# Optimization experiments

Hardware: AMD Instinct MI355X
Metric: run time of the kernel (lower is better)

The kernel has to match this reference:

```python
import jax, jax.numpy as jnp
import numpy as np

D_MODEL = 2048
NUM_HEADS = 16
D_K = D_MODEL // NUM_HEADS
ROPE_THETA = 10000.0


def apply_rope(x, token_positions):
    # x: [B, H, S, D_k]; token_positions: [S] int
    d = x.shape[-1]
    inv_freq = 1.0 / (ROPE_THETA ** (jnp.arange(0, d, 2, dtype=jnp.float32) / d))  # [D_k/2]
    ang = token_positions.astype(jnp.float32)[:, None] * inv_freq[None, :]  # [S, D_k/2]
    cos = jnp.cos(ang)  # broadcast over B, H
    sin = jnp.sin(ang)
    x1 = x[..., 0::2]
    x2 = x[..., 1::2]
    r1 = x1 * cos - x2 * sin
    r2 = x1 * sin + x2 * cos
    return jnp.stack([r1, r2], axis=-1).reshape(x.shape)


def setup_inputs() -> dict:
    key = jax.random.key(0)
    kx, kq, kk, kv, ko = jax.random.split(key, 5)
    scale = 1.0 / np.sqrt(D_MODEL)
    return {
        "x": jax.random.normal(kx, (2, 2048, D_MODEL), dtype=jnp.float32),
        "token_positions": jnp.arange(2048, dtype=jnp.int32),
        "wq": jax.random.normal(kq, (D_MODEL, D_MODEL), dtype=jnp.float32) * scale,
        "wk": jax.random.normal(kk, (D_MODEL, D_MODEL), dtype=jnp.float32) * scale,
        "wv": jax.random.normal(kv, (D_MODEL, D_MODEL), dtype=jnp.float32) * scale,
        "wo": jax.random.normal(ko, (D_MODEL, D_MODEL), dtype=jnp.float32) * scale,
    }


def reference(x, token_positions, wq, wk, wv, wo):
    B, S, _ = x.shape
    # QKV projections (no bias), split heads -> [B, H, S, D_k]
    def split_heads(t):
        return t.reshape(B, S, NUM_HEADS, D_K).transpose(0, 2, 1, 3)

    q = split_heads(jnp.einsum("bsd,ed->bse", x, wq))
    k = split_heads(jnp.einsum("bsd,ed->bse", x, wk))
    v = split_heads(jnp.einsum("bsd,ed->bse", x, wv))

    q = apply_rope(q, token_positions)
    k = apply_rope(k, token_positions)

    scores = jnp.einsum("bhqd,bhkd->bhqk", q, k) / jnp.sqrt(jnp.float32(D_K))
    causal = jnp.tril(jnp.ones((S, S), dtype=bool))  # True where attend allowed
    scores = jnp.where(causal, scores, jnp.float32(-1e9))
    attn = jax.nn.softmax(scores, axis=-1)
    out = jnp.einsum("bhqk,bhkd->bhqd", attn, v)  # [B, H, S, D_k]
    out = out.transpose(0, 2, 1, 3).reshape(B, S, D_MODEL)
    return jnp.einsum("bsd,ed->bse", out, wo)
```

## Files before the change

kernel.cpp:

```cpp
#include <hip/hip_runtime.h>
#include <hip/hip_bf16.h>
#include <math.h>

#define D_MODEL 2048
#define NHEAD   16
#define DK      128
#define SEQ     2048
#define BATCH   2
#define MROWS   (BATCH*SEQ)

typedef __attribute__((ext_vector_type(8))) short short8;
typedef __attribute__((ext_vector_type(4))) short shortx4;
typedef __attribute__((ext_vector_type(4))) float f32x4;

static __device__ __forceinline__ short f2bf(float v) {
    union { __hip_bfloat16 b; short s; } u;
    u.b = __float2bfloat16(v);
    return u.s;
}
static __device__ __forceinline__ float bf2f(short s) {
    union { short s; __hip_bfloat16 b; } u;
    u.s = s;
    return __bfloat162float(u.b);
}

__global__ __launch_bounds__(256) void split_bf16(const float* __restrict__ in,
                                                  short* __restrict__ hi,
                                                  short* __restrict__ lo, int n8)
{
    int i = blockIdx.x * 256 + threadIdx.x;
    const int stride = gridDim.x * 256;
    for (; i < n8; i += stride) {
        const float4 a = ((const float4*)in)[2 * i];
        const float4 b = ((const float4*)in)[2 * i + 1];
        const float f[8] = {a.x, a.y, a.z, a.w, b.x, b.y, b.z, b.w};
        short8 h, l;
#pragma unroll
        for (int e = 0; e < 8; ++e) {
            const short hb = f2bf(f[e]); h[e] = hb; l[e] = f2bf(f[e] - bf2f(hb));
        }
        ((short8*)hi)[i] = h;
        ((short8*)lo)[i] = l;
    }
}

#define GBM 128
#define GBN 128
#define GBK 32
#define LDKG 40

__global__ __launch_bounds__(256, 2) void gemm_nt_bf(const short* __restrict__ Ahg,
                                                     const short* __restrict__ Alg,
                                                     const short* __restrict__ Whg,
                                                     const short* __restrict__ Wlg,
                                                     float* __restrict__ C,
                                                     int M, int N, int K)
{
    __shared__ __align__(16) short Ah[GBM][LDKG];
    __shared__ __align__(16) short Al[GBM][LDKG];
    __shared__ __align__(16) short Bh[GBN][LDKG];
    __shared__ __align__(16) short Bl[GBN][LDKG];

    const int tid  = threadIdx.x;
    const int lane = tid & 63;
    const int w    = tid >> 6;
    const int wm   = (w & 1) * 64;
    const int wn   = (w >> 1) * 64;
    const int l16  = lane & 15;
    const int kb   = (lane >> 4) * 8;

    const size_t row0 = (size_t)blockIdx.y * GBM;
    const size_t col0 = (size_t)blockIdx.x * GBN;

    const int sr0 = tid >> 2;
    const int sr1 = sr0 + 64;
    const int skc = (tid & 3) * 8;

    f32x4 acc[4][4];
#pragma unroll
    for (int i = 0; i < 4; ++i)
#pragma unroll
        for (int j = 0; j < 4; ++j) acc[i][j] = (f32x4)0.0f;

    short8 ra0h = *(const short8*)(Ahg + (row0 + sr0) * K + skc);
    short8 ra0l = *(const short8*)(Alg + (row0 + sr0) * K + skc);
    short8 ra1h = *(const short8*)(Ahg + (row0 + sr1) * K + skc);
    short8 ra1l = *(const short8*)(Alg + (row0 + sr1) * K + skc);
    short8 rw0h = *(const short8*)(Whg + (col0 + sr0) * K + skc);
    short8 rw0l = *(const short8*)(Wlg + (col0 + sr0) * K + skc);
    short8 rw1h = *(const short8*)(Whg + (col0 + sr1) * K + skc);
    short8 rw1l = *(const short8*)(Wlg + (col0 + sr1) * K + skc);

    for (int kt = 0; kt < K; kt += GBK) {
        *(short8*)&Ah[sr0][skc] = ra0h;  *(short8*)&Al[sr0][skc] = ra0l;
        *(short8*)&Ah[sr1][skc] = ra1h;  *(short8*)&Al[sr1][skc] = ra1l;
        *(short8*)&Bh[sr0][skc] = rw0h;  *(short8*)&Bl[sr0][skc] = rw0l;
        *(short8*)&Bh[sr1][skc] = rw1h;  *(short8*)&Bl[sr1][skc] = rw1l;
        __syncthreads();

        if (kt + GBK < K) {
            const int kn = kt + GBK;
            ra0h = *(const short8*)(Ahg + (row0 + sr0) * K + kn + skc);
            ra0l = *(const short8*)(Alg + (row0 + sr0) * K + kn + skc);
            ra1h = *(const short8*)(Ahg + (row0 + sr1) * K + kn + skc);
            ra1l = *(const short8*)(Alg + (row0 + sr1) * K + kn + skc);
            rw0h = *(const short8*)(Whg + (col0 + sr0) * K + kn + skc);
            rw0l = *(const short8*)(Wlg + (col0 + sr0) * K + kn + skc);
            rw1h = *(const short8*)(Whg + (col0 + sr1) * K + kn + skc);
            rw1l = *(const short8*)(Wlg + (col0 + sr1) * K + kn + skc);
        }

        short8 bh[4], bl[4];
#pragma unroll
        for (int fn = 0; fn < 4; ++fn) {
            bh[fn] = *(const short8*)&Bh[wn + fn * 16 + l16][kb];
            bl[fn] = *(const short8*)&Bl[wn + fn * 16 + l16][kb];
        }
#pragma unroll
        for (int fm = 0; fm < 4; ++fm) {
            const short8 ah = *(const short8*)&Ah[wm + fm * 16 + l16][kb];
            const short8 al = *(const short8*)&Al[wm + fm * 16 + l16][kb];
#pragma unroll
            for (int fn = 0; fn < 4; ++fn) {
                acc[fm][fn] = __builtin_amdgcn_mfma_f32_16x16x32_bf16(ah, bh[fn], acc[fm][fn], 0, 0, 0);
                acc[fm][fn] = __builtin_amdgcn_mfma_f32_16x16x32_bf16(ah, bl[fn], acc[fm][fn], 0, 0, 0);
                acc[fm][fn] = __builtin_amdgcn_mfma_f32_16x16x32_bf16(al, bh[fn], acc[fm][fn], 0, 0, 0);
            }
        }
        __syncthreads();
    }

#pragma unroll
    for (int fm = 0; fm < 4; ++fm) {
#pragma unroll
        for (int j = 0; j < 4; ++j) {
            const size_t r = row0 + wm + fm * 16 + (lane >> 4) * 4 + j;
#pragma unroll
            for (int fn = 0; fn < 4; ++fn)
                C[r * N + col0 + wn + fn * 16 + l16] = acc[fm][fn][j];
        }
    }
}

__global__ __launch_bounds__(256, 2) void gemm_nt_mfma(const float* __restrict__ A,
                                                       const float* __restrict__ W,
                                                       float* __restrict__ C,
                                                       int M, int N, int K)
{
    __shared__ __align__(16) short Ah[GBM][LDKG];
    __shared__ __align__(16) short Al[GBM][LDKG];
    __shared__ __align__(16) short Bh[GBN][LDKG];
    __shared__ __align__(16) short Bl[GBN][LDKG];

    const int tid  = threadIdx.x;
    const int lane = tid & 63;
    const int w    = tid >> 6;
    const int wm   = (w & 1) * 64;
    const int wn   = (w >> 1) * 64;
    const int l16  = lane & 15;
    const int kb   = (lane >> 4) * 8;

    const size_t row0 = (size_t)blockIdx.y * GBM;
    const size_t col0 = (size_t)blockIdx.x * GBN;

    const int sr0 = tid >> 2;
    const int sr1 = sr0 + 64;
    const int skc = (tid & 3) * 8;

    f32x4 acc[4][4];
#pragma unroll
    for (int i = 0; i < 4; ++i)
#pragma unroll
        for (int j = 0; j < 4; ++j) acc[i][j] = (f32x4)0.0f;

    float4 pa0a = *(const float4*)(A + (row0 + sr0) * K + skc);
    float4 pa0b = *(const float4*)(A + (row0 + sr0) * K + skc + 4);
    float4 pa1a = *(const float4*)(A + (row0 + sr1) * K + skc);
    float4 pa1b = *(const float4*)(A + (row0 + sr1) * K + skc + 4);
    float4 pw0a = *(const float4*)(W + (col0 + sr0) * K + skc);
    float4 pw0b = *(const float4*)(W + (col0 + sr0) * K + skc + 4);
    float4 pw1a = *(const float4*)(W + (col0 + sr1) * K + skc);
    float4 pw1b = *(const float4*)(W + (col0 + sr1) * K + skc + 4);

    for (int kt = 0; kt < K; kt += GBK) {
        {
            float f[8]; short8 h, l;
#define CVT8(va, vb)                                                        \
            f[0]=va.x; f[1]=va.y; f[2]=va.z; f[3]=va.w;                     \
            f[4]=vb.x; f[5]=vb.y; f[6]=vb.z; f[7]=vb.w;                     \
            _Pragma("unroll")                                               \
            for (int j = 0; j < 8; ++j) {                                   \
                short hb = f2bf(f[j]); h[j] = hb; l[j] = f2bf(f[j] - bf2f(hb)); \
            }
            CVT8(pa0a, pa0b)
            *(short8*)&Ah[sr0][skc] = h;  *(short8*)&Al[sr0][skc] = l;
            CVT8(pa1a, pa1b)
            *(short8*)&Ah[sr1][skc] = h;  *(short8*)&Al[sr1][skc] = l;
            CVT8(pw0a, pw0b)
            *(short8*)&Bh[sr0][skc] = h;  *(short8*)&Bl[sr0][skc] = l;
            CVT8(pw1a, pw1b)
            *(short8*)&Bh[sr1][skc] = h;  *(short8*)&Bl[sr1][skc] = l;
#undef CVT8
        }
        __syncthreads();

        if (kt + GBK < K) {
            const int kn = kt + GBK;
            pa0a = *(const float4*)(A + (row0 + sr0) * K + kn + skc);
            pa0b = *(const float4*)(A + (row0 + sr0) * K + kn + skc + 4);
            pa1a = *(const float4*)(A + (row0 + sr1) * K + kn + skc);
            pa1b = *(const float4*)(A + (row0 + sr1) * K + kn + skc + 4);
            pw0a = *(const float4*)(W + (col0 + sr0) * K + kn + skc);
            pw0b = *(const float4*)(W + (col0 + sr0) * K + kn + skc + 4);
            pw1a = *(const float4*)(W + (col0 + sr1) * K + kn + skc);
            pw1b = *(const float4*)(W + (col0 + sr1) * K + kn + skc + 4);
        }

        short8 bh[4], bl[4];
#pragma unroll
        for (int fn = 0; fn < 4; ++fn) {
            bh[fn] = *(const short8*)&Bh[wn + fn * 16 + l16][kb];
            bl[fn] = *(const short8*)&Bl[wn + fn * 16 + l16][kb];
        }
#pragma unroll
        for (int fm = 0; fm < 4; ++fm) {
            const short8 ah = *(const short8*)&Ah[wm + fm * 16 + l16][kb];
            const short8 al = *(const short8*)&Al[wm + fm * 16 + l16][kb];
#pragma unroll
            for (int fn = 0; fn < 4; ++fn) {
                acc[fm][fn] = __builtin_amdgcn_mfma_f32_16x16x32_bf16(ah, bh[fn], acc[fm][fn], 0, 0, 0);
                acc[fm][fn] = __builtin_amdgcn_mfma_f32_16x16x32_bf16(ah, bl[fn], acc[fm][fn], 0, 0, 0);
                acc[fm][fn] = __builtin_amdgcn_mfma_f32_16x16x32_bf16(al, bh[fn], acc[fm][fn], 0, 0, 0);
            }
        }
        __syncthreads();
    }

#pragma unroll
    for (int fm = 0; fm < 4; ++fm) {
#pragma unroll
        for (int j = 0; j < 4; ++j) {
            const size_t r = row0 + wm + fm * 16 + (lane >> 4) * 4 + j;
#pragma unroll
            for (int fn = 0; fn < 4; ++fn)
                C[r * N + col0 + wn + fn * 16 + l16] = acc[fm][fn][j];
        }
    }
}

__global__ __launch_bounds__(256) void rope_kernel(float* __restrict__ q,
                                                   float* __restrict__ k,
                                                   const int* __restrict__ pos)
{
    const int idx = blockIdx.x * 256 + threadIdx.x;
    if (idx >= MROWS * 1024) return;
    const int pair = idx & 1023;
    const int row  = idx >> 10;
    const int s    = row & (SEQ - 1);
    const int j    = pair & 63;

    const float inv_freq = (float)pow(10000.0, -(double)(2 * j) / 128.0);
    const float ang = (float)pos[s] * inv_freq;
    float sn, cs;
    sincosf(ang, &sn, &cs);

    const size_t off = (size_t)row * D_MODEL + pair * 2;
    float2 vq = *(float2*)(q + off);
    float2 vk = *(float2*)(k + off);
    float2 rq, rk;
    rq.x = vq.x * cs - vq.y * sn;  rq.y = vq.x * sn + vq.y * cs;
    rk.x = vk.x * cs - vk.y * sn;  rk.y = vk.x * sn + vk.y * cs;
    *(float2*)(q + off) = rq;
    *(float2*)(k + off) = rk;
}

#define ABM 128
#define AWQ 32
#define KVT 64
#define KROW 128
#define VLD 72

__device__ __forceinline__ void attn_issue_loads(const float* __restrict__ K,
                                                 const float* __restrict__ V,
                                                 size_t base, int kv0, int tid,
                                                 float4* kreg, float4* vreg)
{
    const int r  = tid >> 2;
    const int d0 = (tid & 3) * 32;
    const float* ksrc = K + base + (size_t)(kv0 + r) * D_MODEL + d0;
#pragma unroll
    for (int u = 0; u < 4; ++u) {
        kreg[2 * u]     = *(const float4*)(ksrc + u * 8);
        kreg[2 * u + 1] = *(const float4*)(ksrc + u * 8 + 4);
    }
#pragma unroll
    for (int it = 0; it < 2; ++it) {
        const int tt  = tid + it * 256;
        const int dq  = tt & 31;
        const int kvq = tt >> 5;
        const float* vs = V + base + (size_t)(kv0 + kvq * 4) * D_MODEL + dq * 4;
#pragma unroll
        for (int i = 0; i < 4; ++i)
            vreg[it * 4 + i] = *(const float4*)(vs + i * D_MODEL);
    }
}

__device__ __forceinline__ void attn_convert_write(short* __restrict__ KhS,
                                                   short* __restrict__ KlS,
                                                   short* __restrict__ VTh,
                                                   short* __restrict__ VTl,
                                                   int tid,
                                                   const float4* kreg,
                                                   const float4* vreg)
{
    const int r = tid >> 2;
#pragma unroll
    for (int u = 0; u < 4; ++u) {
        const float4 f0 = kreg[2 * u];
        const float4 f1 = kreg[2 * u + 1];
        const float f[8] = {f0.x, f0.y, f0.z, f0.w, f1.x, f1.y, f1.z, f1.w};
        short8 hh, ll;
#pragma unroll
        for (int e = 0; e < 8; ++e) {
            const short hb = f2bf(f[e]); hh[e] = hb; ll[e] = f2bf(f[e] - bf2f(hb));
        }
        const int off = r * KROW + (((4 * (tid & 3) + u) ^ (r & 7)) << 3);
        *(short8*)&KhS[off] = hh;
        *(short8*)&KlS[off] = ll;
    }
#pragma unroll
    for (int it = 0; it < 2; ++it) {
        const int tt  = tid + it * 256;
        const int dq  = tt & 31;
        const int kvq = tt >> 5;
        const float4 r0 = vreg[it * 4 + 0];
        const float4 r1 = vreg[it * 4 + 1];
        const float4 r2 = vreg[it * 4 + 2];
        const float4 r3 = vreg[it * 4 + 3];
        const float vals[4][4] = {{r0.x, r0.y, r0.z, r0.w}, {r1.x, r1.y, r1.z, r1.w},
                                  {r2.x, r2.y, r2.z, r2.w}, {r3.x, r3.y, r3.z, r3.w}};
#pragma unroll
        for (int c = 0; c < 4; ++c) {
            const int rr  = dq * 4 + c;
            const int sw  = ((rr >> 2) ^ (rr >> 4)) & 3;
            const int off = rr * VLD + (((kvq >> 1) ^ sw) << 3) + ((kvq & 1) << 2);
            shortx4 hh, ll;
#pragma unroll
            for (int i = 0; i < 4; ++i) {
                const float fv = vals[i][c];
                const short hb = f2bf(fv); hh[i] = hb; ll[i] = f2bf(fv - bf2f(hb));
            }
            *(shortx4*)&VTh[off] = hh;
            *(shortx4*)&VTl[off] = ll;
        }
    }
}

__device__ __forceinline__ void attn_load_q(const float* __restrict__ Q, size_t base,
                                            int qw0, int l16, int g,
                                            short8 qh[2][4], short8 ql[2][4])
{
#pragma unroll
    for (int fq = 0; fq < 2; ++fq)
#pragma unroll
        for (int ks = 0; ks < 4; ++ks) {
            const float* src = Q + base + (size_t)(qw0 + fq * 16 + l16) * D_MODEL + g * 8 + ks * 32;
            const float4 f0 = *(const float4*)src;
            const float4 f1 = *(const float4*)(src + 4);
            const float f[8] = {f0.x, f0.y, f0.z, f0.w, f1.x, f1.y, f1.z, f1.w};
            short8 hh, ll;
#pragma unroll
            for (int e = 0; e < 8; ++e) {
                const short hb = f2bf(f[e]); hh[e] = hb; ll[e] = f2bf(f[e] - bf2f(hb));
            }
            qh[fq][ks] = hh; ql[fq][ks] = ll;
        }
}

__device__ __forceinline__ void attn_write_o(float* __restrict__ O, size_t base,
                                             int qw0, int g, int l16,
                                             const f32x4 accO[2][8], const float lstate[2])
{
    float rl[2][4];
#pragma unroll
    for (int fm = 0; fm < 2; ++fm)
#pragma unroll
        for (int j = 0; j < 4; ++j)
            rl[fm][j] = 1.0f / __shfl(lstate[fm], (g << 2) | j);
#pragma unroll
    for (int fm = 0; fm < 2; ++fm)
#pragma unroll
        for (int j = 0; j < 4; ++j) {
            const size_t row = base + (size_t)(qw0 + fm * 16 + 4 * g + j) * D_MODEL;
#pragma unroll
            for (int fd = 0; fd < 8; ++fd)
                O[row + fd * 16 + l16] = accO[fm][fd][j] * rl[fm][j];
        }
}

__global__ __launch_bounds__(256, 1) void flash_attn_mfma(const float* __restrict__ Q,
                                                          const float* __restrict__ K,
                                                          const float* __restrict__ V,
                                                          float* __restrict__ O)
{
    __shared__ __align__(16) short KhS[2][KVT * KROW];
    __shared__ __align__(16) short KlS[2][KVT * KROW];
    __shared__ __align__(16) short VTh[2][DK * VLD];
    __shared__ __align__(16) short VTl[2][DK * VLD];

    const int tid  = threadIdx.x;
    const int lane = tid & 63;
    const int w    = tid >> 6;
    const int l16  = lane & 15;
    const int g    = lane >> 4;
    const int h    = blockIdx.y & (NHEAD - 1);
    const int b    = blockIdx.y >> 4;
    const size_t base = (size_t)b * SEQ * D_MODEL + (size_t)h * DK;
    const float scale = 0.08838834764831845f;

    const int qtA = blockIdx.x;
    const int qtB = 15 - qtA;
    const int ntA = 2 * qtA + 2;
    const int total = 34;

    short8 qh[2][4], ql[2][4];
    attn_load_q(Q, base, qtA * ABM + w * AWQ, l16, g, qh, ql);

    f32x4 accO[2][8];
#pragma unroll
    for (int i = 0; i < 2; ++i)
#pragma unroll
        for (int j = 0; j < 8; ++j) accO[i][j] = (f32x4)0.0f;
    float mstate[2] = {-3.0e38f, -3.0e38f};
    float lstate[2] = {0.f, 0.f};

    float4 kreg[8], vreg[8];
    attn_issue_loads(K, V, base, 0, tid, kreg, vreg);
    attn_convert_write(KhS[0], KlS[0], VTh[0], VTl[0], tid, kreg, vreg);
    int cur = 0;

    for (int st = 0; st < total; ++st) {
        const int pass = (st >= ntA) ? 1 : 0;
        const int t    = pass ? (st - ntA) : st;
        const int qt   = pass ? qtB : qtA;
        const int kv0  = t * KVT;
        const int qw0  = qt * ABM + w * AWQ;

        __syncthreads();

        if (st + 1 < total) {
            const int t2 = (st + 1 >= ntA) ? (st + 1 - ntA) : (st + 1);
            attn_issue_loads(K, V, base, t2 * KVT, tid, kreg, vreg);
        }

        if (pass && t == 0) {
            attn_write_o(O, base, qtA * ABM + w * AWQ, g, l16, accO, lstate);
            attn_load_q(Q, base, qtB * ABM + w * AWQ, l16, g, qh, ql);
#pragma unroll
            for (int i = 0; i < 2; ++i)
#pragma unroll
                for (int j = 0; j < 8; ++j) accO[i][j] = (f32x4)0.0f;
            mstate[0] = mstate[1] = -3.0e38f;
            lstate[0] = lstate[1] = 0.f;
        }

        const bool active = (kv0 <= qw0 + AWQ - 1);
        if (active) {
            f32x4 accS[4][2];
#pragma unroll
            for (int i = 0; i < 4; ++i) { accS[i][0] = (f32x4)0.0f; accS[i][1] = (f32x4)0.0f; }
#pragma unroll
            for (int ks = 0; ks < 4; ++ks) {
#pragma unroll
                for (int fs = 0; fs < 4; ++fs) {
                    const int koff = (fs * 16 + l16) * KROW + (((g + 4 * ks) ^ (l16 & 7)) << 3);
                    const short8 kh = *(const short8*)&KhS[cur][koff];
                    const short8 kl = *(const short8*)&KlS[cur][koff];
#pragma unroll
                    for (int fq = 0; fq < 2; ++fq) {
                        accS[fs][fq] = __builtin_amdgcn_mfma_f32_16x16x32_bf16(kh, qh[fq][ks], accS[fs][fq], 0, 0, 0);
                        accS[fs][fq] = __builtin_amdgcn_mfma_f32_16x16x32_bf16(kh, ql[fq][ks], accS[fs][fq], 0, 0, 0);
                        accS[fs][fq] = __builtin_amdgcn_mfma_f32_16x16x32_bf16(kl, qh[fq][ks], accS[fs][fq], 0, 0, 0);
                    }
                }
            }

            const bool needmask = (kv0 + KVT - 1 > qw0);
            float al[2];
#pragma unroll
            for (int fq = 0; fq < 2; ++fq) {
                const int qg = qw0 + fq * 16 + l16;
                float mx = -3.0e38f;
#pragma unroll
                for (int fs = 0; fs < 4; ++fs)
#pragma unroll
                    for (int j = 0; j < 4; ++j) {
                        float s = accS[fs][fq][j] * scale;
                        if (needmask) {
                            const int kvg = kv0 + fs * 16 + g * 4 + j;
                            s = (kvg <= qg) ? s : -3.0e38f;
                        }
                        accS[fs][fq][j] = s;
                        mx = fmaxf(mx, s);
                    }
                mx = fmaxf(mx, __shfl_xor(mx, 16));
                mx = fmaxf(mx, __shfl_xor(mx, 32));
                const float mnew = fmaxf(mstate[fq], mx);
                al[fq] = __expf(mstate[fq] - mnew);
                mstate[fq] = mnew;
                float sm = 0.f;
#pragma unroll
                for (int fs = 0; fs < 4; ++fs)
#pragma unroll
                    for (int j = 0; j < 4; ++j) {
                        const float p = __expf(accS[fs][fq][j] - mnew);
                        accS[fs][fq][j] = p;
                        sm += p;
                    }
                sm += __shfl_xor(sm, 16);
                sm += __shfl_xor(sm, 32);
                lstate[fq] = lstate[fq] * al[fq] + sm;
            }

            float alr[2][4];
#pragma unroll
            for (int fm = 0; fm < 2; ++fm)
#pragma unroll
                for (int j = 0; j < 4; ++j)
                    alr[fm][j] = __shfl(al[fm], (g << 2) | j);
#pragma unroll
            for (int fm = 0; fm < 2; ++fm)
#pragma unroll
                for (int fd = 0; fd < 8; ++fd)
#pragma unroll
                    for (int j = 0; j < 4; ++j)
                        accO[fm][fd][j] *= alr[fm][j];

#pragma unroll
            for (int ks = 0; ks < 2; ++ks) {
                short8 pah[2], pal[2];
#pragma unroll
                for (int fm = 0; fm < 2; ++fm) {
                    float pv[8];
#pragma unroll
                    for (int e = 0; e < 8; ++e) {
                        const int j = e & 3;
                        const int srcl = ((((lane >> 4) & 1) << 1) + (e >> 2)) * 16 + l16;
                        const float c0 = __shfl(accS[2 * ks][fm][j], srcl);
                        const float c1 = __shfl(accS[2 * ks + 1][fm][j], srcl);
                        pv[e] = (g >> 1) ? c1 : c0;
                    }
                    short8 hh, ll;
#pragma unroll
                    for (int e = 0; e < 8; ++e) {
                        const short hb = f2bf(pv[e]); hh[e] = hb; ll[e] = f2bf(pv[e] - bf2f(hb));
                    }
                    pah[fm] = hh; pal[fm] = ll;
                }
#pragma unroll
                for (int fd = 0; fd < 8; ++fd) {
                    const int r = fd * 16 + l16;
                    const int sw = ((r >> 2) ^ (r >> 4)) & 3;
                    const int off = r * VLD + (((g + 4 * ks) ^ sw) << 3);
                    const short8 vh = *(const short8*)&VTh[cur][off];
                    const short8 vl = *(const short8*)&VTl[cur][off];
#pragma unroll
                    for (int fm = 0; fm < 2; ++fm) {
                        accO[fm][fd] = __builtin_amdgcn_mfma_f32_16x16x32_bf16(pah[fm], vh, accO[fm][fd], 0, 0, 0);
                        accO[fm][fd] = __builtin_amdgcn_mfma_f32_16x16x32_bf16(pah[fm], vl, accO[fm][fd], 0, 0, 0);
                        accO[fm][fd] = __builtin_amdgcn_mfma_f32_16x16x32_bf16(pal[fm], vh, accO[fm][fd], 0, 0, 0);
                    }
                }
            }
        }

        if (st + 1 < total)
            attn_convert_write(KhS[cur ^ 1], KlS[cur ^ 1], VTh[cur ^ 1], VTl[cur ^ 1], tid, kreg, vreg);
        cur ^= 1;
    }

    attn_write_o(O, base, qtB * ABM + w * AWQ, g, l16, accO, lstate);
}

extern "C" void kernel_launch(void* const* d_in, const int* in_sizes, int n_in,
                              void* d_out, int out_size, void* d_ws, size_t ws_size,
                              hipStream_t stream)
{
    const float* x  = (const float*)d_in[0];
    const int*  pos = (const int*)d_in[1];
    const float* wq = (const float*)d_in[2];
    const float* wk = (const float*)d_in[3];
    const float* wv = (const float*)d_in[4];
    const float* wo = (const float*)d_in[5];
    float* out = (float*)d_out;

    char* base = (char*)d_ws;
    const size_t MB = 1024ull * 1024ull;
    float* q  = (float*)(base + 0 * MB);
    float* k  = (float*)(base + 32 * MB);
    float* v  = (float*)(base + 64 * MB);
    float* ao = (float*)(base + 96 * MB);

    const dim3 blk(256);
    const dim3 ggrid(D_MODEL / GBN, MROWS / GBM);
    const dim3 agrid(SEQ / (2 * ABM), BATCH * NHEAD);

    const bool presplit = (ws_size >= 224 * MB);

    if (presplit) {
        short* xh  = (short*)(base + 128 * MB);
        short* xl  = (short*)(base + 144 * MB);
        short* wqh = (short*)(base + 160 * MB);
        short* wql = (short*)(base + 168 * MB);
        short* wkh = (short*)(base + 176 * MB);
        short* wkl = (short*)(base + 184 * MB);
        short* wvh = (short*)(base + 192 * MB);
        short* wvl = (short*)(base + 200 * MB);
        short* woh = (short*)(base + 208 * MB);
        short* wol = (short*)(base + 216 * MB);
        short* aoh = xh;
        short* aol = xl;

        const int nx8 = MROWS * D_MODEL / 8;
        const int nw8 = D_MODEL * D_MODEL / 8;
        split_bf16<<<2048, blk, 0, stream>>>(x,  xh,  xl,  nx8);
        split_bf16<<<2048, blk, 0, stream>>>(wq, wqh, wql, nw8);
        split_bf16<<<2048, blk, 0, stream>>>(wk, wkh, wkl, nw8);
        split_bf16<<<2048, blk, 0, stream>>>(wv, wvh, wvl, nw8);
        split_bf16<<<2048, blk, 0, stream>>>(wo, woh, wol, nw8);

        gemm_nt_bf<<<ggrid, blk, 0, stream>>>(xh, xl, wqh, wql, q, MROWS, D_MODEL, D_MODEL);
        gemm_nt_bf<<<ggrid, blk, 0, stream>>>(xh, xl, wkh, wkl, k, MROWS, D_MODEL, D_MODEL);
        gemm_nt_bf<<<ggrid, blk, 0, stream>>>(xh, xl, wvh, wvl, v, MROWS, D_MODEL, D_MODEL);

        rope_kernel<<<(MROWS * 1024 + 255) / 256, blk, 0, stream>>>(q, k, pos);

        flash_attn_mfma<<<agrid, blk, 0, stream>>>(q, k, v, ao);

        split_bf16<<<2048, blk, 0, stream>>>(ao, aoh, aol, nx8);
        gemm_nt_bf<<<ggrid, blk, 0, stream>>>(aoh, aol, woh, wol, out, MROWS, D_MODEL, D_MODEL);
    } else {
        gemm_nt_mfma<<<ggrid, blk, 0, stream>>>(x, wq, q, MROWS, D_MODEL, D_MODEL);
        gemm_nt_mfma<<<ggrid, blk, 0, stream>>>(x, wk, k, MROWS, D_MODEL, D_MODEL);
        gemm_nt_mfma<<<ggrid, blk, 0, stream>>>(x, wv, v, MROWS, D_MODEL, D_MODEL);

        rope_kernel<<<(MROWS * 1024 + 255) / 256, blk, 0, stream>>>(q, k, pos);

        flash_attn_mfma<<<agrid, blk, 0, stream>>>(q, k, v, ao);

        gemm_nt_mfma<<<ggrid, blk, 0, stream>>>(ao, wo, out, MROWS, D_MODEL, D_MODEL);
    }
}
```

Measured before the change: 836.7 us.

## Use 8 waves per attention block with 16 query rows each

The flash attention kernel moves from 4 waves each owning 32 query rows to 8 waves (512 threads) each owning 16 rows. This halves per-wave accumulator and Q register state and doubles the waves available to hide latency. The K/V tile loading is split across more threads, and V high/low conversion is divided between the two halves of the block, with a new LDS swizzle for the transposed V. In exchange, each K/V fragment read from LDS now feeds half as many MFMAs, and the larger block raises synchronisation cost.

```diff
diff --git a/kernel.cpp b/kernel.cpp
--- a/kernel.cpp
+++ b/kernel.cpp
@@ -10,7 +10,6 @@
 #define MROWS   (BATCH*SEQ)
 
 typedef __attribute__((ext_vector_type(8))) short short8;
-typedef __attribute__((ext_vector_type(4))) short shortx4;
 typedef __attribute__((ext_vector_type(4))) float f32x4;
 
 static __device__ __forceinline__ short f2bf(float v) {
@@ -275,7 +274,6 @@
 }
 
 #define ABM 128
-#define AWQ 32
 #define KVT 64
 #define KROW 128
 #define VLD 72
@@ -285,24 +283,19 @@
                                                  size_t base, int kv0, int tid,
                                                  float4* kreg, float4* vreg)
 {
-    const int r  = tid >> 2;
-    const int d0 = (tid & 3) * 32;
-    const float* ksrc = K + base + (size_t)(kv0 + r) * D_MODEL + d0;
-#pragma unroll
-    for (int u = 0; u < 4; ++u) {
-        kreg[2 * u]     = *(const float4*)(ksrc + u * 8);
-        kreg[2 * u + 1] = *(const float4*)(ksrc + u * 8 + 4);
-    }
-#pragma unroll
-    for (int it = 0; it < 2; ++it) {
-        const int tt  = tid + it * 256;
-        const int dq  = tt & 31;
-        const int kvq = tt >> 5;
-        const float* vs = V + base + (size_t)(kv0 + kvq * 4) * D_MODEL + dq * 4;
-#pragma unroll
-        for (int i = 0; i < 4; ++i)
-            vreg[it * 4 + i] = *(const float4*)(vs + i * D_MODEL);
-    }
+    const int r  = tid >> 3;
+    const int j7 = tid & 7;
+    const float* ksrc = K + base + (size_t)(kv0 + r) * D_MODEL + j7 * 16;
+#pragma unroll
+    for (int u = 0; u < 4; ++u)
+        kreg[u] = *(const float4*)(ksrc + u * 4);
+
+    const int dq  = tid & 31;
+    const int kvo = (tid >> 5) & 7;
+    const float* vs = V + base + (size_t)(kv0 + kvo * 8) * D_MODEL + dq * 4;
+#pragma unroll
+    for (int i = 0; i < 8; ++i)
+        vreg[i] = *(const float4*)(vs + i * D_MODEL);
 }
 
 __device__ __forceinline__ void attn_convert_write(short* __restrict__ KhS,
@@ -313,9 +306,10 @@
                                                    const float4* kreg,
                                                    const float4* vreg)
 {
-    const int r = tid >> 2;
-#pragma unroll
-    for (int u = 0; u < 4; ++u) {
+    const int r  = tid >> 3;
+    const int j7 = tid & 7;
+#pragma unroll
+    for (int u = 0; u < 2; ++u) {
         const float4 f0 = kreg[2 * u];
         const float4 f1 = kreg[2 * u + 1];
         const float f[8] = {f0.x, f0.y, f0.z, f0.w, f1.x, f1.y, f1.z, f1.w};
@@ -324,81 +318,72 @@
         for (int e = 0; e < 8; ++e) {
             const short hb = f2bf(f[e]); hh[e] = hb; ll[e] = f2bf(f[e] - bf2f(hb));
         }
-        const int off = r * KROW + (((4 * (tid & 3) + u) ^ (r & 7)) << 3);
+        const int v   = j7 * 2 + u;
+        const int off = r * KROW + ((v ^ (r & 7)) << 3);
         *(short8*)&KhS[off] = hh;
         *(short8*)&KlS[off] = ll;
     }
-#pragma unroll
-    for (int it = 0; it < 2; ++it) {
-        const int tt  = tid + it * 256;
-        const int dq  = tt & 31;
-        const int kvq = tt >> 5;
-        const float4 r0 = vreg[it * 4 + 0];
-        const float4 r1 = vreg[it * 4 + 1];
-        const float4 r2 = vreg[it * 4 + 2];
-        const float4 r3 = vreg[it * 4 + 3];
-        const float vals[4][4] = {{r0.x, r0.y, r0.z, r0.w}, {r1.x, r1.y, r1.z, r1.w},
-                                  {r2.x, r2.y, r2.z, r2.w}, {r3.x, r3.y, r3.z, r3.w}};
-#pragma unroll
-        for (int c = 0; c < 4; ++c) {
-            const int rr  = dq * 4 + c;
-            const int sw  = ((rr >> 2) ^ (rr >> 4)) & 3;
-            const int off = rr * VLD + (((kvq >> 1) ^ sw) << 3) + ((kvq & 1) << 2);
-            shortx4 hh, ll;
-#pragma unroll
-            for (int i = 0; i < 4; ++i) {
-                const float fv = vals[i][c];
-                const short hb = f2bf(fv); hh[i] = hb; ll[i] = f2bf(fv - bf2f(hb));
+
+    const int dq  = tid & 31;
+    const int kvo = (tid >> 5) & 7;
+    const bool isLo = (tid >= 256);
+#pragma unroll
+    for (int c = 0; c < 4; ++c) {
+        short8 s;
+#pragma unroll
+        for (int i = 0; i < 8; ++i) {
+            const float fv = ((const float*)&vreg[i])[c];
+            if (isLo) {
+                const short hb = f2bf(fv);
+                s[i] = f2bf(fv - bf2f(hb));
+            } else {
+                s[i] = f2bf(fv);
             }
-            *(shortx4*)&VTh[off] = hh;
-            *(shortx4*)&VTl[off] = ll;
-        }
+        }
+        const int rr  = dq * 4 + c;
+        const int off = rr * VLD + ((kvo ^ (dq & 7)) << 3);
+        if (isLo) *(short8*)&VTl[off] = s;
+        else      *(short8*)&VTh[off] = s;
     }
 }
 
 __device__ __forceinline__ void attn_load_q(const float* __restrict__ Q, size_t base,
                                             int qw0, int l16, int g,
-                                            short8 qh[2][4], short8 ql[2][4])
-{
-#pragma unroll
-    for (int fq = 0; fq < 2; ++fq)
-#pragma unroll
-        for (int ks = 0; ks < 4; ++ks) {
-            const float* src = Q + base + (size_t)(qw0 + fq * 16 + l16) * D_MODEL + g * 8 + ks * 32;
-            const float4 f0 = *(const float4*)src;
-            const float4 f1 = *(const float4*)(src + 4);
-            const float f[8] = {f0.x, f0.y, f0.z, f0.w, f1.x, f1.y, f1.z, f1.w};
-            short8 hh, ll;
-#pragma unroll
-            for (int e = 0; e < 8; ++e) {
-                const short hb = f2bf(f[e]); hh[e] = hb; ll[e] = f2bf(f[e] - bf2f(hb));
-            }
-            qh[fq][ks] = hh; ql[fq][ks] = ll;
-        }
+                                            short8 qh[4], short8 ql[4])
+{
+#pragma unroll
+    for (int ks = 0; ks < 4; ++ks) {
+        const float* src = Q + base + (size_t)(qw0 + l16) * D_MODEL + g * 8 + ks * 32;
+        const float4 f0 = *(const float4*)src;
+        const float4 f1 = *(const float4*)(src + 4);
+        const float f[8] = {f0.x, f0.y, f0.z, f0.w, f1.x, f1.y, f1.z, f1.w};
+        short8 hh, ll;
+#pragma unroll
+        for (int e = 0; e < 8; ++e) {
+            const short hb = f2bf(f[e]); hh[e] = hb; ll[e] = f2bf(f[e] - bf2f(hb));
+        }
+        qh[ks] = hh; ql[ks] = ll;
+    }
 }
 
 __device__ __forceinline__ void attn_write_o(float* __restrict__ O, size_t base,
                                              int qw0, int g, int l16,
-                                             const f32x4 accO[2][8], const float lstate[2])
-{
-    float rl[2][4];
-#pragma unroll
-    for (int fm = 0; fm < 2; ++fm)
-#pragma unroll
-        for (int j = 0; j < 4; ++j)
-            rl[fm][j] = 1.0f / __shfl(lstate[fm], (g << 2) | j);
-#pragma unroll
-    for (int fm = 0; fm < 2; ++fm)
-#pragma unroll
-        for (int j = 0; j < 4; ++j) {
-            const size_t row = base + (size_t)(qw0 + fm * 16 + 4 * g + j) * D_MODEL;
-#pragma unroll
-            for (int fd = 0; fd < 8; ++fd)
-                O[row + fd * 16 + l16] = accO[fm][fd][j] * rl[fm][j];
-        }
-}
-
-__global__ __launch_bounds__(256, 1) void flash_attn_mfma(const float* __restrict__ Q,
+                                             const f32x4 accO[8], float lstate)
+{
+    float rl[4];
+#pragma unroll
+    for (int j = 0; j < 4; ++j)
+        rl[j] = 1.0f / __shfl(lstate, (g << 2) | j);
+#pragma unroll
+    for (int j = 0; j < 4; ++j) {
+        const size_t row = base + (size_t)(qw0 + 4 * g + j) * D_MODEL;
+#pragma unroll
+        for (int fd = 0; fd < 8; ++fd)
+            O[row + fd * 16 + l16] = accO[fd][j] * rl[j];
+    }
+}
+
+__global__ __launch_bounds__(512, 1) void flash_attn_mfma(const float* __restrict__ Q,
                                                           const float* __restrict__ K,
                                                           const float* __restrict__ V,
                                                           float* __restrict__ O)
@@ -423,18 +408,16 @@
     const int ntA = 2 * qtA + 2;
     const int total = 34;
 
-    short8 qh[2][4], ql[2][4];
-    attn_load_q(Q, base, qtA * ABM + w * AWQ, l16, g, qh, ql);
-
-    f32x4 accO[2][8];
-#pragma unroll
-    for (int i = 0; i < 2; ++i)
-#pragma unroll
-        for (int j = 0; j < 8; ++j) accO[i][j] = (f32x4)0.0f;
-    float mstate[2] = {-3.0e38f, -3.0e38f};
-    float lstate[2] = {0.f, 0.f};
-
-    float4 kreg[8], vreg[8];
+    short8 qh[4], ql[4];
+    attn_load_q(Q, base, qtA * ABM + w * 16, l16, g, qh, ql);
+
+    f32x4 accO[8];
+#pragma unroll
+    for (int j = 0; j < 8; ++j) accO[j] = (f32x4)0.0f;
+    float mstate = -3.0e38f;
+    float lstate = 0.f;
+
+    float4 kreg[4], vreg[8];
     attn_issue_loads(K, V, base, 0, tid, kreg, vreg);
     attn_convert_write(KhS[0], KlS[0], VTh[0], VTl[0], tid, kreg, vreg);
     int cur = 0;
@@ -444,7 +427,7 @@
         const int t    = pass ? (st - ntA) : st;
         const int qt   = pass ? qtB : qtA;
         const int kv0  = t * KVT;
-        const int qw0  = qt * ABM + w * AWQ;
+        const int qw0  = qt * ABM + w * 16;
 
         __syncthreads();
 
@@ -454,21 +437,19 @@
         }
 
         if (pass && t == 0) {
-            attn_write_o(O, base, qtA * ABM + w * AWQ, g, l16, accO, lstate);
-            attn_load_q(Q, base, qtB * ABM + w * AWQ, l16, g, qh, ql);
-#pragma unroll
-            for (int i = 0; i < 2; ++i)
-#pragma unroll
-                for (int j = 0; j < 8; ++j) accO[i][j] = (f32x4)0.0f;
-            mstate[0] = mstate[1] = -3.0e38f;
-            lstate[0] = lstate[1] = 0.f;
-        }
-
-        const bool active = (kv0 <= qw0 + AWQ - 1);
+            attn_write_o(O, base, qtA * ABM + w * 16, g, l16, accO, lstate);
+            attn_load_q(Q, base, qtB * ABM + w * 16, l16, g, qh, ql);
+#pragma unroll
+            for (int j = 0; j < 8; ++j) accO[j] = (f32x4)0.0f;
+            mstate = -3.0e38f;
+            lstate = 0.f;
+        }
+
+        const bool active = (kv0 <= qw0 + 15);
         if (active) {
-            f32x4 accS[4][2];
-#pragma unroll
-            for (int i = 0; i < 4; ++i) { accS[i][0] = (f32x4)0.0f; accS[i][1] = (f32x4)0.0f; }
+            f32x4 accS[4];
+#pragma unroll
+            for (int i = 0; i < 4; ++i) accS[i] = (f32x4)0.0f;
 #pragma unroll
             for (int ks = 0; ks < 4; ++ks) {
 #pragma unroll
@@ -476,100 +457,80 @@
                     const int koff = (fs * 16 + l16) * KROW + (((g + 4 * ks) ^ (l16 & 7)) << 3);
                     const short8 kh = *(const short8*)&KhS[cur][koff];
                     const short8 kl = *(const short8*)&KlS[cur][koff];
-#pragma unroll
-                    for (int fq = 0; fq < 2; ++fq) {
-                        accS[fs][fq] = __builtin_amdgcn_mfma_f32_16x16x32_bf16(kh, qh[fq][ks], accS[fs][fq], 0, 0, 0);
-                        accS[fs][fq] = __builtin_amdgcn_mfma_f32_16x16x32_bf16(kh, ql[fq][ks], accS[fs][fq], 0, 0, 0);
-                        accS[fs][fq] = __builtin_amdgcn_mfma_f32_16x16x32_bf16(kl, qh[fq][ks], accS[fs][fq], 0, 0, 0);
-                    }
+                    accS[fs] = __builtin_amdgcn_mfma_f32_16x16x32_bf16(kh, qh[ks], accS[fs], 0, 0, 0);
+                    accS[fs] = __builtin_amdgcn_mfma_f32_16x16x32_bf16(kh, ql[ks], accS[fs], 0, 0, 0);
+                    accS[fs] = __builtin_amdgcn_mfma_f32_16x16x32_bf16(kl, qh[ks], accS[fs], 0, 0, 0);
                 }
             }
 
             const bool needmask = (kv0 + KVT - 1 > qw0);
-            float al[2];
-#pragma unroll
-            for (int fq = 0; fq < 2; ++fq) {
-                const int qg = qw0 + fq * 16 + l16;
-                float mx = -3.0e38f;
-#pragma unroll
-                for (int fs = 0; fs < 4; ++fs)
-#pragma unroll
-                    for (int j = 0; j < 4; ++j) {
-                        float s = accS[fs][fq][j] * scale;
-                        if (needmask) {
-                            const int kvg = kv0 + fs * 16 + g * 4 + j;
-                            s = (kvg <= qg) ? s : -3.0e38f;
-                        }
-                        accS[fs][fq][j] = s;
-                        mx = fmaxf(mx, s);
+            const int qg = qw0 + l16;
+            float mx = -3.0e38f;
+#pragma unroll
+            for (int fs = 0; fs < 4; ++fs)
+#pragma unroll
+                for (int j = 0; j < 4; ++j) {
+                    float s = accS[fs][j] * scale;
+                    if (needmask) {
+                        const int kvg = kv0 + fs * 16 + g * 4 + j;
+                        s = (kvg <= qg) ? s : -3.0e38f;
                     }
-                mx = fmaxf(mx, __shfl_xor(mx, 16));
-                mx = fmaxf(mx, __shfl_xor(mx, 32));
-                const float mnew = fmaxf(mstate[fq], mx);
-                al[fq] = __expf(mstate[fq] - mnew);
-                mstate[fq] = mnew;
-                float sm = 0.f;
-#pragma unroll
-                for (int fs = 0; fs < 4; ++fs)
-#pragma unroll
-                    for (int j = 0; j < 4; ++j) {
-                        const float p = __expf(accS[fs][fq][j] - mnew);
-                        accS[fs][fq][j] = p;
-                        sm += p;
-                    }
-                sm += __shfl_xor(sm, 16);
-                sm += __shfl_xor(sm, 32);
-                lstate[fq] = lstate[fq] * al[fq] + sm;
-            }
-
-            float alr[2][4];
-#pragma unroll
-            for (int fm = 0; fm < 2; ++fm)
+                    accS[fs][j] = s;
+                    mx = fmaxf(mx, s);
+                }
+            mx = fmaxf(mx, __shfl_xor(mx, 16));
+            mx = fmaxf(mx, __shfl_xor(mx, 32));
+            const float mnew = fmaxf(mstate, mx);
+            const float al = __expf(mstate - mnew);
+            mstate = mnew;
+            float sm = 0.f;
+#pragma unroll
+            for (int fs = 0; fs < 4; ++fs)
+#pragma unroll
+                for (int j = 0; j < 4; ++j) {
+                    const float p = __expf(accS[fs][j] - mnew);
+                    accS[fs][j] = p;
+                    sm += p;
+                }
+            sm += __shfl_xor(sm, 16);
+            sm += __shfl_xor(sm, 32);
+            lstate = lstate * al + sm;
+
+            float alr[4];
+#pragma unroll
+            for (int j = 0; j < 4; ++j)
+                alr[j] = __shfl(al, (g << 2) | j);
+#pragma unroll
+            for (int fd = 0; fd < 8; ++fd)
 #pragma unroll
                 for (int j = 0; j < 4; ++j)
-                    alr[fm][j] = __shfl(al[fm], (g << 2) | j);
-#pragma unroll
-            for (int fm = 0; fm < 2; ++fm)
-#pragma unroll
-                for (int fd = 0; fd < 8; ++fd)
-#pragma unroll
-                    for (int j = 0; j < 4; ++j)
-                        accO[fm][fd][j] *= alr[fm][j];
+                    accO[fd][j] *= alr[j];
 
 #pragma unroll
             for (int ks = 0; ks < 2; ++ks) {
-                short8 pah[2], pal[2];
-#pragma unroll
-                for (int fm = 0; fm < 2; ++fm) {
-                    float pv[8];
-#pragma unroll
-                    for (int e = 0; e < 8; ++e) {
-                        const int j = e & 3;
-                        const int srcl = ((((lane >> 4) & 1) << 1) + (e >> 2)) * 16 + l16;
-                        const float c0 = __shfl(accS[2 * ks][fm][j], srcl);
-                        const float c1 = __shfl(accS[2 * ks + 1][fm][j], srcl);
-                        pv[e] = (g >> 1) ? c1 : c0;
-                    }
-                    short8 hh, ll;
-#pragma unroll
-                    for (int e = 0; e < 8; ++e) {
-                        const short hb = f2bf(pv[e]); hh[e] = hb; ll[e] = f2bf(pv[e] - bf2f(hb));
-                    }
-                    pah[fm] = hh; pal[fm] = ll;
+                float pv[8];
+#pragma unroll
+                for (int e = 0; e < 8; ++e) {
+                    const int j = e & 3;
+                    const int srcl = (((g & 1) << 1) + (e >> 2)) * 16 + l16;
+                    const float c0 = __shfl(accS[2 * ks][j], srcl);
+                    const float c1 = __shfl(accS[2 * ks + 1][j], srcl);
+                    pv[e] = (g >> 1) ? c1 : c0;
+                }
+                short8 pah, pal;
+#pragma unroll
+                for (int e = 0; e < 8; ++e) {
+                    const short hb = f2bf(pv[e]); pah[e] = hb; pal[e] = f2bf(pv[e] - bf2f(hb));
                 }
 #pragma unroll
                 for (int fd = 0; fd < 8; ++fd) {
                     const int r = fd * 16 + l16;
-                    const int sw = ((r >> 2) ^ (r >> 4)) & 3;
-                    const int off = r * VLD + (((g + 4 * ks) ^ sw) << 3);
+                    const int off = r * VLD + (((4 * ks + g) ^ ((r >> 2) & 7)) << 3);
                     const short8 vh = *(const short8*)&VTh[cur][off];
                     const short8 vl = *(const short8*)&VTl[cur][off];
-#pragma unroll
-                    for (int fm = 0; fm < 2; ++fm) {
-                        accO[fm][fd] = __builtin_amdgcn_mfma_f32_16x16x32_bf16(pah[fm], vh, accO[fm][fd], 0, 0, 0);
-                        accO[fm][fd] = __builtin_amdgcn_mfma_f32_16x16x32_bf16(pah[fm], vl, accO[fm][fd], 0, 0, 0);
-                        accO[fm][fd] = __builtin_amdgcn_mfma_f32_16x16x32_bf16(pal[fm], vh, accO[fm][fd], 0, 0, 0);
-                    }
+                    accO[fd] = __builtin_amdgcn_mfma_f32_16x16x32_bf16(pah, vh, accO[fd], 0, 0, 0);
+                    accO[fd] = __builtin_amdgcn_mfma_f32_16x16x32_bf16(pah, vl, accO[fd], 0, 0, 0);
+                    accO[fd] = __builtin_amdgcn_mfma_f32_16x16x32_bf16(pal, vh, accO[fd], 0, 0, 0);
                 }
             }
         }
@@ -579,7 +540,7 @@
         cur ^= 1;
     }
 
-    attn_write_o(O, base, qtB * ABM + w * AWQ, g, l16, accO, lstate);
+    attn_write_o(O, base, qtB * ABM + w * 16, g, l16, accO, lstate);
 }
 
 extern "C" void kernel_launch(void* const* d_in, const int* in_sizes, int n_in,
@@ -602,6 +563,7 @@
     float* ao = (float*)(base + 96 * MB);
 
     const dim3 blk(256);
+    const dim3 ablk(512);
     const dim3 ggrid(D_MODEL / GBN, MROWS / GBM);
     const dim3 agrid(SEQ / (2 * ABM), BATCH * NHEAD);
 
@@ -635,7 +597,7 @@
 
         rope_kernel<<<(MROWS * 1024 + 255) / 256, blk, 0, stream>>>(q, k, pos);
 
-        flash_attn_mfma<<<agrid, blk, 0, stream>>>(q, k, v, ao);
+        flash_attn_mfma<<<agrid, ablk, 0, stream>>>(q, k, v, ao);
 
         split_bf16<<<2048, blk, 0, stream>>>(ao, aoh, aol, nx8);
         gemm_nt_bf<<<ggrid, blk, 0, stream>>>(aoh, aol, woh, wol, out, MROWS, D_MODEL, D_MODEL);
@@ -646,7 +608,7 @@
 
         rope_kernel<<<(MROWS * 1024 + 255) / 256, blk, 0, stream>>>(q, k, pos);
 
-        flash_attn_mfma<<<agrid, blk, 0, stream>>>(q, k, v, ao);
+        flash_attn_mfma<<<agrid, ablk, 0, stream>>>(q, k, v, ao);
 
         gemm_nt_mfma<<<ggrid, blk, 0, stream>>>(ao, wo, out, MROWS, D_MODEL, D_MODEL);
     }
```

New measurement: 779.8 us. 1.07x faster.
